# Optimization experiments

Hardware: AMD Instinct MI355X
Metric: run time of the kernel (lower is better)

## Reference

```python
import jax, jax.numpy as jnp
import numpy as np

B, L, D_MODEL = 1, 2048, 1024
D_STATE, D_CONV, EXPAND = 16, 4, 2
D_INNER = EXPAND * D_MODEL          # 2048
DT_RANK = D_MODEL // 16             # 64
I_SIZE = 4 * D_MODEL                # 4096
EPS = 1e-6


def setup_inputs() -> dict:
    key = jax.random.key(0)
    ks = jax.random.split(key, 24)
    s = 0.02
    inp = {
        "hidden_states": jax.random.normal(ks[0], (B, L, D_MODEL), jnp.float32),
        "attention_mask": jnp.ones((B, L), jnp.float32),
        "mnorm_w": jnp.ones((D_MODEL,), jnp.float32),
        "ln1_w": jnp.ones((D_MODEL,), jnp.float32),
        "ln2_w": jnp.ones((D_MODEL,), jnp.float32),
        "gate_w": jax.random.normal(ks[1], (I_SIZE, D_MODEL), jnp.float32) * s,
        "up_w": jax.random.normal(ks[2], (I_SIZE, D_MODEL), jnp.float32) * s,
        "down_w": jax.random.normal(ks[3], (D_MODEL, I_SIZE), jnp.float32) * s,
    }
    a_log = jnp.log(jnp.broadcast_to(jnp.arange(1, D_STATE + 1, dtype=jnp.float32), (D_INNER, D_STATE)))
    i = 4
    for d in ("f", "b"):
        inp[f"in_w_{d}"] = jax.random.normal(ks[i], (2 * D_INNER, D_MODEL), jnp.float32) * s; i += 1
        inp[f"conv_w_{d}"] = jax.random.normal(ks[i], (D_INNER, D_CONV), jnp.float32) * s; i += 1
        inp[f"conv_b_{d}"] = jnp.zeros((D_INNER,), jnp.float32)
        inp[f"xproj_w_{d}"] = jax.random.normal(ks[i], (DT_RANK + 2 * D_STATE, D_INNER), jnp.float32) * s; i += 1
        inp[f"dt_w_{d}"] = jax.random.normal(ks[i], (D_INNER, DT_RANK), jnp.float32) * s; i += 1
        inp[f"dt_b_{d}"] = jax.random.normal(ks[i], (D_INNER,), jnp.float32) * 0.1; i += 1
        inp[f"A_log_{d}"] = a_log
        inp[f"Dp_{d}"] = jnp.ones((D_INNER,), jnp.float32)
        inp[f"out_w_{d}"] = jax.random.normal(ks[i], (D_MODEL, D_INNER), jnp.float32) * s; i += 1
    return inp


def rmsnorm(x, w, eps=EPS):
    xf = x.astype(jnp.float32)
    var = jnp.mean(xf * xf, axis=-1, keepdims=True)
    return w * (xf * jax.lax.rsqrt(var + eps)).astype(x.dtype)


def depthwise_causal_conv(x, w, b):
    # x: [B,L,C], w: [C,K] -> causal depthwise conv, output [B,L,C]
    xt = jnp.transpose(x, (0, 2, 1))                      # [B,C,L]
    k = w[:, None, :]                                     # [C,1,K] (OIL)
    y = jax.lax.conv_general_dilated(
        xt, k, window_strides=(1,), padding=[(D_CONV - 1, 0)],
        dimension_numbers=("NCL", "OIL", "NCL"), feature_group_count=D_INNER)
    return jnp.transpose(y + b[None, :, None], (0, 2, 1))


def selective_scan(u, dt, Bm, Cm, A):
    # u, dt: [B,L,Di]; Bm, Cm: [B,L,N]; A: [Di,N]
    def step(h, inp):
        dt_t, B_t, C_t, u_t = inp                         # [B,Di],[B,N],[B,N],[B,Di]
        dA = jnp.exp(dt_t[:, :, None] * A)                # [B,Di,N]
        h = dA * h + (dt_t * u_t)[:, :, None] * B_t[:, None, :]
        y = jnp.einsum("bdn,bn->bd", h, C_t)
        return h, y
    h0 = jnp.zeros((u.shape[0], A.shape[0], A.shape[1]), u.dtype)
    xs = (jnp.swapaxes(dt, 0, 1), jnp.swapaxes(Bm, 0, 1), jnp.swapaxes(Cm, 0, 1), jnp.swapaxes(u, 0, 1))
    _, ys = jax.lax.scan(step, h0, xs)                    # ys: [L,B,Di]
    return jnp.swapaxes(ys, 0, 1)


def mamba_dir(x, in_w, conv_w, conv_b, xproj_w, dt_w, dt_b, A_log, Dp, out_w):
    xz = x @ in_w.T                                       # [B,L,2*Di]
    xi, z = jnp.split(xz, 2, axis=-1)
    xc = jax.nn.silu(depthwise_causal_conv(xi, conv_w, conv_b))
    dbc = xc @ xproj_w.T                                  # [B,L,dt_rank+2N]
    dt_raw = dbc[..., :DT_RANK]
    Bm = dbc[..., DT_RANK:DT_RANK + D_STATE]
    Cm = dbc[..., DT_RANK + D_STATE:]
    dt = jax.nn.softplus(dt_raw @ dt_w.T + dt_b)          # [B,L,Di]
    A = -jnp.exp(A_log)
    y = selective_scan(xc, dt, Bm, Cm, A) + xc * Dp
    y = y * jax.nn.silu(z)
    return y @ out_w.T


def reference(hidden_states, attention_mask,
              in_w_f, conv_w_f, conv_b_f, xproj_w_f, dt_w_f, dt_b_f, A_log_f, Dp_f, out_w_f,
              in_w_b, conv_w_b, conv_b_b, xproj_w_b, dt_w_b, dt_b_b, A_log_b, Dp_b, out_w_b,
              mnorm_w, ln1_w, ln2_w, gate_w, up_w, down_w):
    x = hidden_states
    h = rmsnorm(x, ln1_w) * attention_mask[..., None]
    y_f = mamba_dir(h, in_w_f, conv_w_f, conv_b_f, xproj_w_f, dt_w_f, dt_b_f, A_log_f, Dp_f, out_w_f)
    y_b = jnp.flip(mamba_dir(jnp.flip(h, axis=1), in_w_b, conv_w_b, conv_b_b, xproj_w_b,
                             dt_w_b, dt_b_b, A_log_b, Dp_b, out_w_b), axis=1)
    x = x + rmsnorm(y_f + y_b, mnorm_w)                   # fuse='add' + block RMSNorm, residual
    h2 = rmsnorm(x, ln2_w)
    mlp = (jax.nn.silu(h2 @ gate_w.T) * (h2 @ up_w.T)) @ down_w.T
    return x + mlp
```

## Files before the change

kernel.cpp:

```cpp
#include <hip/hip_runtime.h>

#define L_SEQ 2048
#define DMODEL 1024
#define DINNER 2048
#define DSTATE 16
#define DTRANK 64
#define DBC_LD 96
#define NC 64
#define TC 32
#define DCAT 4096
#define XZLD 8192
#define LS96 (L_SEQ * 96)

typedef __bf16 bf16x8 __attribute__((ext_vector_type(8)));
typedef __bf16 bf16x4 __attribute__((ext_vector_type(4)));
typedef float f32x4 __attribute__((ext_vector_type(4)));

__device__ __forceinline__ void gload_lds16(const void* g, void* l) {
    __builtin_amdgcn_global_load_lds(
        (const __attribute__((address_space(1))) void*)g,
        (__attribute__((address_space(3))) void*)l, 16, 0, 0);
}

template<int EPI>
__global__ __launch_bounds__(256) void gemm16(
    const __bf16* __restrict__ A, const __bf16* __restrict__ W,
    float* __restrict__ C, const float* __restrict__ aux, __bf16* __restrict__ Cb,
    int M, int N, int K, int lda, int ldb, int ldc, int kSplit)
{
    __shared__ __bf16 lsA[128 * 64];
    __shared__ __bf16 lsB[128 * 64];
    const int tid  = threadIdx.x;
    const int lane = tid & 63;
    const int wave = tid >> 6;
    const int wr = wave >> 1, wc = wave & 1;
    const int m0 = blockIdx.x * 128, n0 = blockIdx.y * 128;
    const int kz = blockIdx.z;
    const int Kc = K / kSplit;
    const int q  = lane & 7;
    const int rb = wave * 32 + (lane >> 3);

    f32x4 acc[4][4] = {};

    for (int k0 = kz * Kc; k0 < kz * Kc + Kc; k0 += 64) {
        #pragma unroll
        for (int i = 0; i < 4; ++i) {
            const int row = rb + i * 8;
            const int sk  = (q * 8) ^ ((row & 7) << 3);
            gload_lds16(A + (size_t)(m0 + row) * lda + k0 + sk,
                        &lsA[(wave * 4 + i) * 512]);
            int rw = n0 + row; rw = rw < N ? rw : N - 1;
            gload_lds16(W + (size_t)rw * ldb + k0 + sk,
                        &lsB[(wave * 4 + i) * 512]);
        }
        __syncthreads();
        #pragma unroll
        for (int kk = 0; kk < 2; ++kk) {
            bf16x8 af[4], bf[4];
            #pragma unroll
            for (int m = 0; m < 4; ++m) {
                const int row = wr * 64 + m * 16 + (lane & 15);
                const int kb  = (kk * 32 + (lane >> 4) * 8) ^ ((row & 7) << 3);
                af[m] = *(const bf16x8*)&lsA[row * 64 + kb];
            }
            #pragma unroll
            for (int n = 0; n < 4; ++n) {
                const int row = wc * 64 + n * 16 + (lane & 15);
                const int kb  = (kk * 32 + (lane >> 4) * 8) ^ ((row & 7) << 3);
                bf[n] = *(const bf16x8*)&lsB[row * 64 + kb];
            }
            #pragma unroll
            for (int m = 0; m < 4; ++m)
            #pragma unroll
            for (int n = 0; n < 4; ++n)
                acc[m][n] = __builtin_amdgcn_mfma_f32_16x16x32_bf16(af[m], bf[n], acc[m][n], 0, 0, 0);
        }
        __syncthreads();
    }

    float* Cout = (EPI == 5) ? C + (size_t)kz * M * ldc : C;
    const int cr = (lane >> 4) * 4, cc = lane & 15;
    #pragma unroll
    for (int mi = 0; mi < 4; ++mi)
    #pragma unroll
    for (int ni = 0; ni < 4; ++ni) {
        const int c = n0 + wc * 64 + ni * 16 + cc;
        if (c >= N) continue;
        #pragma unroll
        for (int g = 0; g < 4; ++g) {
            const int r = m0 + wr * 64 + mi * 16 + cr + g;
            float v = acc[mi][ni][g];
            if (EPI == 1) {
                float xv = v + aux[c];
                Cout[(size_t)r * ldc + c] = (xv > 20.f) ? xv : log1pf(__expf(xv));
            } else if (EPI == 6) {
                const int rr = (c < (N >> 1)) ? r : (M - 1 - r);
                Cb[(size_t)rr * ldc + c] = (__bf16)v;
            } else {
                Cout[(size_t)r * ldc + c] = v;
            }
        }
    }
}

__global__ __launch_bounds__(256) void gemm_mlp(
    const __bf16* __restrict__ A, const __bf16* __restrict__ Wg,
    const __bf16* __restrict__ Wu, __bf16* __restrict__ m16,
    int M, int N, int K, int lda, int ldb, int ldm)
{
    __shared__ __bf16 lsA[128 * 64];
    __shared__ __bf16 lsB[128 * 64];
    const int tid  = threadIdx.x;
    const int lane = tid & 63;
    const int wave = tid >> 6;
    const int wr = wave >> 1, wc = wave & 1;
    const int m0 = blockIdx.x * 128, n0 = blockIdx.y * 64;
    const int q  = lane & 7;
    const int rb = wave * 32 + (lane >> 3);

    f32x4 acc[4][4] = {};

    for (int k0 = 0; k0 < K; k0 += 64) {
        #pragma unroll
        for (int i = 0; i < 4; ++i) {
            const int row = rb + i * 8;
            const int sk  = (q * 8) ^ ((row & 7) << 3);
            gload_lds16(A + (size_t)(m0 + row) * lda + k0 + sk,
                        &lsA[(wave * 4 + i) * 512]);
            const __bf16* src = (row < 64) ? Wg + (size_t)(n0 + row) * ldb
                                           : Wu + (size_t)(n0 + row - 64) * ldb;
            gload_lds16(src + k0 + sk, &lsB[(wave * 4 + i) * 512]);
        }
        __syncthreads();
        #pragma unroll
        for (int kk = 0; kk < 2; ++kk) {
            bf16x8 af[4], bf[4];
            #pragma unroll
            for (int m = 0; m < 4; ++m) {
                const int row = wr * 64 + m * 16 + (lane & 15);
                const int kb  = (kk * 32 + (lane >> 4) * 8) ^ ((row & 7) << 3);
                af[m] = *(const bf16x8*)&lsA[row * 64 + kb];
            }
            #pragma unroll
            for (int n = 0; n < 4; ++n) {
                const int row = wc * 32 + (n & 1) * 16 + (n >> 1) * 64 + (lane & 15);
                const int kb  = (kk * 32 + (lane >> 4) * 8) ^ ((row & 7) << 3);
                bf[n] = *(const bf16x8*)&lsB[row * 64 + kb];
            }
            #pragma unroll
            for (int m = 0; m < 4; ++m)
            #pragma unroll
            for (int n = 0; n < 4; ++n)
                acc[m][n] = __builtin_amdgcn_mfma_f32_16x16x32_bf16(af[m], bf[n], acc[m][n], 0, 0, 0);
        }
        __syncthreads();
    }

    const int cr = (lane >> 4) * 4, cc = lane & 15;
    #pragma unroll
    for (int mi = 0; mi < 4; ++mi)
    #pragma unroll
    for (int nn = 0; nn < 2; ++nn) {
        const int c = n0 + wc * 32 + nn * 16 + cc;
        #pragma unroll
        for (int g = 0; g < 4; ++g) {
            const int r = m0 + wr * 64 + mi * 16 + cr + g;
            const float gv = acc[mi][nn][g];
            const float uv = acc[mi][nn + 2][g];
            m16[(size_t)r * ldm + c] = (__bf16)(gv / (1.f + __expf(-gv)) * uv);
        }
    }
}

#define NJOBS 9
struct CvtJobs {
    const float* src[NJOBS];
    __bf16* dst[NJOBS];
    int cum[NJOBS + 1];
};
__global__ __launch_bounds__(256) void cvt_multi(CvtJobs j, int total8) {
    const int g = blockIdx.x * 256 + threadIdx.x;
    if (g >= total8) return;
    for (int i = 0; i < NJOBS; ++i) {
        if (g < j.cum[i + 1]) {
            const int off = (g - j.cum[i]) * 8;
            const float4 a = *(const float4*)(j.src[i] + off);
            const float4 b = *(const float4*)(j.src[i] + off + 4);
            bf16x8 o;
            o[0]=(__bf16)a.x; o[1]=(__bf16)a.y; o[2]=(__bf16)a.z; o[3]=(__bf16)a.w;
            o[4]=(__bf16)b.x; o[5]=(__bf16)b.y; o[6]=(__bf16)b.z; o[7]=(__bf16)b.w;
            *(bf16x8*)(j.dst[i] + off) = o;
            return;
        }
    }
}

__global__ __launch_bounds__(256) void cvt_outw(
    const float* __restrict__ wf, const float* __restrict__ wb, __bf16* __restrict__ dst)
{
    const int g = blockIdx.x * 256 + threadIdx.x;
    const int half = g >> 18;
    const int i = (g & 262143) * 8;
    const int r = i >> 11, c = i & 2047;
    const float* src = (half ? wb : wf) + (size_t)r * 2048 + c;
    const float4 a = *(const float4*)src;
    const float4 b = *(const float4*)(src + 4);
    bf16x8 o;
    o[0]=(__bf16)a.x; o[1]=(__bf16)a.y; o[2]=(__bf16)a.z; o[3]=(__bf16)a.w;
    o[4]=(__bf16)b.x; o[5]=(__bf16)b.y; o[6]=(__bf16)b.z; o[7]=(__bf16)b.w;
    *(bf16x8*)(dst + (size_t)r * 4096 + half * 2048 + c) = o;
}

__global__ __launch_bounds__(256) void rmsnorm_mask_kernel(
    const float* __restrict__ x, const float* __restrict__ w, const float* __restrict__ mask,
    __bf16* __restrict__ h16)
{
    __shared__ float sred[4];
    const int row = blockIdx.x, t = threadIdx.x;
    float4 v = ((const float4*)(x + (size_t)row * DMODEL))[t];
    float ss = v.x*v.x + v.y*v.y + v.z*v.z + v.w*v.w;
    #pragma unroll
    for (int m = 1; m < 64; m <<= 1) ss += __shfl_xor(ss, m);
    if ((t & 63) == 0) sred[t >> 6] = ss;
    __syncthreads();
    ss = sred[0] + sred[1] + sred[2] + sred[3];
    const float scale = rsqrtf(ss * (1.f / DMODEL) + 1e-6f) * mask[row];
    float4 wv = ((const float4*)w)[t];
    bf16x4 o;
    o[0] = (__bf16)(v.x * wv.x * scale); o[1] = (__bf16)(v.y * wv.y * scale);
    o[2] = (__bf16)(v.z * wv.z * scale); o[3] = (__bf16)(v.w * wv.w * scale);
    *(bf16x4*)&h16[(size_t)row * DMODEL + t * 4] = o;
}

__global__ __launch_bounds__(256) void conv_silu_kernel(
    const __bf16* __restrict__ xz,
    const float* __restrict__ w0, const float* __restrict__ b0,
    const float* __restrict__ w1, const float* __restrict__ b1,
    __bf16* __restrict__ xc16)
{
    const int idx = blockIdx.x * 256 + threadIdx.x;
    const int dcat = idx & (DCAT - 1);
    const int t = idx >> 12;
    const int dir = dcat >> 11, dloc = dcat & 2047;
    const float* w = (dir ? w1 : w0) + dloc * 4;
    float acc = (dir ? b1 : b0)[dloc];
    const float4 wv = *(const float4*)w;
    const float wj[4] = {wv.x, wv.y, wv.z, wv.w};
    const __bf16* src = xz + dir * 4096 + dloc;
    #pragma unroll
    for (int jj = 0; jj < 4; ++jj) {
        const int tt = t - 3 + jj;
        if (tt >= 0) acc += wj[jj] * (float)src[(size_t)tt * XZLD];
    }
    xc16[(size_t)idx] = (__bf16)(acc / (1.f + __expf(-acc)));
}

__global__ __launch_bounds__(256) void dbc_finalize(
    const float* __restrict__ P, float* __restrict__ dbc, __bf16* __restrict__ dbc16)
{
    const int i = blockIdx.x * 256 + threadIdx.x;
    const int dir = i / LS96, rem = i - dir * LS96;
    float v = 0.f;
    #pragma unroll
    for (int s = 0; s < 8; ++s) v += P[(size_t)dir * 8 * LS96 + (size_t)s * LS96 + rem];
    dbc[i] = v;
    const int r = rem / 96, c = rem - r * 96;
    if (c < DTRANK) dbc16[(size_t)dir * L_SEQ * DTRANK + r * DTRANK + c] = (__bf16)v;
}

__global__ __launch_bounds__(256) void scan_p1(
    const __bf16* __restrict__ u, const float* __restrict__ dt,
    const float* __restrict__ dbc, const float* __restrict__ A0, const float* __restrict__ A1,
    __bf16* __restrict__ Pb, __bf16* __restrict__ Sb)
{
    __shared__ float sB[TC * 16];
    const int tid = threadIdx.x;
    const int c = blockIdx.x;
    const int dcat = blockIdx.y * 256 + tid;
    const int dir = blockIdx.y >> 3;
    const int dloc = dcat & 2047;
    const int t0 = c * TC;
    const float* dbcD = dbc + (size_t)dir * LS96;
    for (int i = tid; i < TC * 16; i += 256)
        sB[i] = dbcD[(t0 + (i >> 4)) * DBC_LD + DTRANK + (i & 15)];
    __syncthreads();
    const float* Alog = (dir ? A1 : A0) + (size_t)dloc * 16;
    float A[16], h[16], Pa[16];
    #pragma unroll
    for (int n = 0; n < 16; n += 4) {
        const float4 av = *(const float4*)(Alog + n);
        A[n]   = -__expf(av.x); A[n+1] = -__expf(av.y);
        A[n+2] = -__expf(av.z); A[n+3] = -__expf(av.w);
    }
    #pragma unroll
    for (int n = 0; n < 16; ++n) { h[n] = 0.f; Pa[n] = 1.f; }
    #pragma unroll 2
    for (int t = 0; t < TC; ++t) {
        const float dtv = dt[(size_t)(t0 + t) * DCAT + dcat];
        const float du  = dtv * (float)u[(size_t)(t0 + t) * DCAT + dcat];
        #pragma unroll
        for (int n = 0; n < 16; ++n) {
            const float a = __expf(dtv * A[n]);
            h[n] = a * h[n] + du * sB[t * 16 + n];
            Pa[n] *= a;
        }
    }
    __bf16* pp = Pb + ((size_t)c * DCAT + dcat) * 16;
    __bf16* sp = Sb + ((size_t)c * DCAT + dcat) * 16;
    bf16x8 pv0, pv1, sv0, sv1;
    #pragma unroll
    for (int n = 0; n < 8; ++n) {
        pv0[n] = (__bf16)Pa[n]; pv1[n] = (__bf16)Pa[n + 8];
        sv0[n] = (__bf16)h[n];  sv1[n] = (__bf16)h[n + 8];
    }
    *(bf16x8*)pp = pv0; *(bf16x8*)(pp + 8) = pv1;
    *(bf16x8*)sp = sv0; *(bf16x8*)(sp + 8) = sv1;
}

__global__ __launch_bounds__(256) void scan_mid(
    const __bf16* __restrict__ Pb, const __bf16* __restrict__ Sb, __bf16* __restrict__ Hb)
{
    const int i = blockIdx.x * 256 + threadIdx.x;
    float H = 0.f;
    for (int c = 0; c < NC; ++c) {
        Hb[(size_t)c * 65536 + i] = (__bf16)H;
        H = (float)Pb[(size_t)c * 65536 + i] * H + (float)Sb[(size_t)c * 65536 + i];
    }
}

__global__ __launch_bounds__(256) void scan_p3(
    const __bf16* __restrict__ u, const float* __restrict__ dt,
    const float* __restrict__ dbc, const float* __restrict__ A0, const float* __restrict__ A1,
    const float* __restrict__ Dp0, const float* __restrict__ Dp1,
    const __bf16* __restrict__ Hb, const __bf16* __restrict__ xz,
    __bf16* __restrict__ ygcat)
{
    __shared__ float sB[TC * 16], sC[TC * 16];
    const int tid = threadIdx.x;
    const int c = blockIdx.x;
    const int dcat = blockIdx.y * 256 + tid;
    const int dir = blockIdx.y >> 3;
    const int dloc = dcat & 2047;
    const int t0 = c * TC;
    const float* dbcD = dbc + (size_t)dir * LS96;
    for (int i = tid; i < TC * 16; i += 256) {
        sB[i] = dbcD[(t0 + (i >> 4)) * DBC_LD + DTRANK + (i & 15)];
        sC[i] = dbcD[(t0 + (i >> 4)) * DBC_LD + DTRANK + DSTATE + (i & 15)];
    }
    __syncthreads();
    const float* Alog = (dir ? A1 : A0) + (size_t)dloc * 16;
    const __bf16* hp = Hb + ((size_t)c * DCAT + dcat) * 16;
    const bf16x8 hv0 = *(const bf16x8*)hp;
    const bf16x8 hv1 = *(const bf16x8*)(hp + 8);
    float A[16], h[16];
    #pragma unroll
    for (int n = 0; n < 8; ++n) { h[n] = (float)hv0[n]; h[n + 8] = (float)hv1[n]; }
    #pragma unroll
    for (int n = 0; n < 16; n += 4) {
        const float4 av = *(const float4*)(Alog + n);
        A[n]   = -__expf(av.x); A[n+1] = -__expf(av.y);
        A[n+2] = -__expf(av.z); A[n+3] = -__expf(av.w);
    }
    const float Dv = (dir ? Dp1 : Dp0)[dloc];
    const __bf16* zsrc = xz + dir * 4096 + 2048 + dloc;
    #pragma unroll 2
    for (int t = 0; t < TC; ++t) {
        const float dtv = dt[(size_t)(t0 + t) * DCAT + dcat];
        const float uv  = (float)u[(size_t)(t0 + t) * DCAT + dcat];
        const float du  = dtv * uv;
        float y = uv * Dv;
        #pragma unroll
        for (int n = 0; n < 16; ++n) {
            const float a = __expf(dtv * A[n]);
            h[n] = a * h[n] + du * sB[t * 16 + n];
            y += h[n] * sC[t * 16 + n];
        }
        const float zv = (float)zsrc[(size_t)(t0 + t) * XZLD];
        const int orow = dir ? (L_SEQ - 1 - (t0 + t)) : (t0 + t);
        ygcat[(size_t)orow * DCAT + dcat] = (__bf16)(y * (zv / (1.f + __expf(-zv))));
    }
}

__global__ __launch_bounds__(256) void addnorm2_kernel(
    const float* __restrict__ x0, const float* __restrict__ P,
    const float* __restrict__ mw, const float* __restrict__ w2,
    float* __restrict__ x2, __bf16* __restrict__ h2_16)
{
    __shared__ float sred[8];
    const int row = blockIdx.x, t = threadIdx.x;
    const size_t PS = (size_t)L_SEQ * DMODEL;
    float4 yv = ((const float4*)(P + (size_t)row * DMODEL))[t];
    #pragma unroll
    for (int s = 1; s < 4; ++s) {
        float4 pv = ((const float4*)(P + s * PS + (size_t)row * DMODEL))[t];
        yv.x += pv.x; yv.y += pv.y; yv.z += pv.z; yv.w += pv.w;
    }
    float ss = yv.x*yv.x + yv.y*yv.y + yv.z*yv.z + yv.w*yv.w;
    #pragma unroll
    for (int m = 1; m < 64; m <<= 1) ss += __shfl_xor(ss, m);
    if ((t & 63) == 0) sred[t >> 6] = ss;
    __syncthreads();
    const float s1 = sred[0] + sred[1] + sred[2] + sred[3];
    const float sc1 = rsqrtf(s1 * (1.f / DMODEL) + 1e-6f);
    float4 xv = ((const float4*)(x0 + (size_t)row * DMODEL))[t];
    float4 mv = ((const float4*)mw)[t];
    float4 o;
    o.x = xv.x + mv.x * yv.x * sc1; o.y = xv.y + mv.y * yv.y * sc1;
    o.z = xv.z + mv.z * yv.z * sc1; o.w = xv.w + mv.w * yv.w * sc1;
    ((float4*)(x2 + (size_t)row * DMODEL))[t] = o;
    float s2 = o.x*o.x + o.y*o.y + o.z*o.z + o.w*o.w;
    #pragma unroll
    for (int m = 1; m < 64; m <<= 1) s2 += __shfl_xor(s2, m);
    if ((t & 63) == 0) sred[4 + (t >> 6)] = s2;
    __syncthreads();
    const float st = sred[4] + sred[5] + sred[6] + sred[7];
    const float sc2 = rsqrtf(st * (1.f / DMODEL) + 1e-6f);
    float4 wv = ((const float4*)w2)[t];
    bf16x4 o2;
    o2[0] = (__bf16)(wv.x * o.x * sc2); o2[1] = (__bf16)(wv.y * o.y * sc2);
    o2[2] = (__bf16)(wv.z * o.z * sc2); o2[3] = (__bf16)(wv.w * o.w * sc2);
    *(bf16x4*)&h2_16[(size_t)row * DMODEL + t * 4] = o2;
}

__global__ __launch_bounds__(256) void addout_kernel(
    const float* __restrict__ x2, const float* __restrict__ P, float* __restrict__ out)
{
    const size_t i = ((size_t)blockIdx.x * 256 + threadIdx.x) * 4;
    const size_t PS = (size_t)L_SEQ * DMODEL;
    float4 v = *(const float4*)(x2 + i);
    #pragma unroll
    for (int s = 0; s < 4; ++s) {
        const float4 pv = *(const float4*)(P + s * PS + i);
        v.x += pv.x; v.y += pv.y; v.z += pv.z; v.w += pv.w;
    }
    *(float4*)(out + i) = v;
}

extern "C" void kernel_launch(void* const* d_in, const int* in_sizes, int n_in,
                              void* d_out, int out_size, void* d_ws, size_t ws_size,
                              hipStream_t stream)
{
    const float* x       = (const float*)d_in[0];
    const float* mask    = (const float*)d_in[1];
    const float* mnorm_w = (const float*)d_in[2];
    const float* ln1_w   = (const float*)d_in[3];
    const float* ln2_w   = (const float*)d_in[4];
    const float* gate_w  = (const float*)d_in[5];
    const float* up_w    = (const float*)d_in[6];
    const float* down_w  = (const float*)d_in[7];
    const float* in_w[2]    = {(const float*)d_in[8],  (const float*)d_in[17]};
    const float* conv_w[2]  = {(const float*)d_in[9],  (const float*)d_in[18]};
    const float* conv_b[2]  = {(const float*)d_in[10], (const float*)d_in[19]};
    const float* xproj_w[2] = {(const float*)d_in[11], (const float*)d_in[20]};
    const float* dt_w[2]    = {(const float*)d_in[12], (const float*)d_in[21]};
    const float* dt_b[2]    = {(const float*)d_in[13], (const float*)d_in[22]};
    const float* A_log[2]   = {(const float*)d_in[14], (const float*)d_in[23]};
    const float* Dp[2]      = {(const float*)d_in[15], (const float*)d_in[24]};
    const float* out_w[2]   = {(const float*)d_in[16], (const float*)d_in[25]};

    float* ws = (float*)d_ws;
    const size_t MF = 1u << 20;
    __bf16* h16    = (__bf16*)(ws);
    float*  x2     = ws + 1 * MF;
    __bf16* xzcat  = (__bf16*)(ws + 3 * MF);
    __bf16* xc16   = (__bf16*)(ws + 11 * MF);
    float*  dtb    = ws + 15 * MF;
    float*  dbc    = ws + 23 * MF;
    __bf16* dbc16  = (__bf16*)(ws + 23 * MF + 524288);
    __bf16* Pb     = (__bf16*)(ws + 24 * MF);
    __bf16* Sb     = (__bf16*)(ws + 26 * MF);
    float*  dbcP   = ws + 24 * MF;
    __bf16* Hb     = (__bf16*)(ws + 28 * MF);
    __bf16* ygcat  = (__bf16*)(ws + 30 * MF);
    __bf16* h2_16  = (__bf16*)(ws + 34 * MF);
    __bf16* wbase  = (__bf16*)(ws + 35 * MF);
    const size_t M4 = 4u << 20, M2 = 2u << 20;
    __bf16* wINcat  = wbase;
    __bf16* wOUTcat = wbase + 2 * M4;
    __bf16* wG      = wbase + 3 * M4;
    __bf16* wU      = wbase + 4 * M4;
    __bf16* wDN     = wbase + 5 * M4;
    __bf16* wXP[2]  = {wbase + 6 * M4,            wbase + 6 * M4 + 196608};
    __bf16* wDT[2]  = {wbase + 6 * M4 + 393216,   wbase + 6 * M4 + 524288};
    __bf16* mbuf16  = ygcat;
    float*  gemmP   = dtb;

    CvtJobs j;
    const float* srcs[NJOBS] = {in_w[0], in_w[1], gate_w, up_w, down_w,
                                xproj_w[0], xproj_w[1], dt_w[0], dt_w[1]};
    __bf16* dsts[NJOBS] = {wINcat, wINcat + M4, wG, wU, wDN, wXP[0], wXP[1], wDT[0], wDT[1]};
    const int szs[NJOBS] = {4194304, 4194304, 4194304, 4194304, 4194304,
                            196608, 196608, 131072, 131072};
    int cum = 0;
    for (int i = 0; i < NJOBS; ++i) {
        j.src[i] = srcs[i]; j.dst[i] = dsts[i]; j.cum[i] = cum; cum += szs[i] / 8;
    }
    j.cum[NJOBS] = cum;
    cvt_multi<<<(cum + 255) / 256, 256, 0, stream>>>(j, cum);
    cvt_outw<<<(2 * 1024 * 2048 / 8) / 256, 256, 0, stream>>>(out_w[0], out_w[1], wOUTcat);

    rmsnorm_mask_kernel<<<L_SEQ, 256, 0, stream>>>(x, ln1_w, mask, h16);

    gemm16<6><<<dim3(16, 64), 256, 0, stream>>>(
        h16, wINcat, nullptr, nullptr, xzcat, 2048, 8192, 1024, 1024, 1024, 8192, 1);

    conv_silu_kernel<<<(L_SEQ * DCAT) / 256, 256, 0, stream>>>(
        xzcat, conv_w[0], conv_b[0], conv_w[1], conv_b[1], xc16);

    for (int dir = 0; dir < 2; ++dir)
        gemm16<5><<<dim3(16, 1, 8), 256, 0, stream>>>(
            xc16 + dir * 2048, wXP[dir], dbcP + (size_t)dir * 8 * LS96, nullptr, nullptr,
            2048, 96, 2048, 4096, 2048, 96, 8);
    dbc_finalize<<<(2 * LS96) / 256, 256, 0, stream>>>(dbcP, dbc, dbc16);

    for (int dir = 0; dir < 2; ++dir)
        gemm16<1><<<dim3(16, 16), 256, 0, stream>>>(
            dbc16 + (size_t)dir * L_SEQ * DTRANK, wDT[dir], dtb + dir * 2048, dt_b[dir],
            nullptr, 2048, 2048, 64, 64, 64, 4096, 1);

    scan_p1<<<dim3(NC, 16), 256, 0, stream>>>(
        xc16, dtb, dbc, A_log[0], A_log[1], Pb, Sb);
    scan_mid<<<65536 / 256, 256, 0, stream>>>(Pb, Sb, Hb);
    scan_p3<<<dim3(NC, 16), 256, 0, stream>>>(
        xc16, dtb, dbc, A_log[0], A_log[1], Dp[0], Dp[1], Hb, xzcat, ygcat);

    gemm16<5><<<dim3(16, 8, 4), 256, 0, stream>>>(
        ygcat, wOUTcat, gemmP, nullptr, nullptr, 2048, 1024, 4096, 4096, 4096, 1024, 4);
    addnorm2_kernel<<<L_SEQ, 256, 0, stream>>>(x, gemmP, mnorm_w, ln2_w, x2, h2_16);

    gemm_mlp<<<dim3(16, 64), 256, 0, stream>>>(
        h2_16, wG, wU, mbuf16, 2048, 4096, 1024, 1024, 1024, 4096);
    gemm16<5><<<dim3(16, 8, 4), 256, 0, stream>>>(
        mbuf16, wDN, gemmP, nullptr, nullptr, 2048, 1024, 4096, 4096, 4096, 1024, 4);
    addout_kernel<<<(L_SEQ * DMODEL) / (256 * 4), 256, 0, stream>>>(
        x2, gemmP, (float*)d_out);
}
```

Measured before the change: 384.0 us.

## Split GEMM kernels, add XCD-aware block swizzle, store dt in bf16, merge direction launches

The templated GEMM is split into specialized kernels around a shared core. The in-projection, MLP and split-K partial GEMMs now remap block indices so neighbouring tiles land on the same XCD for better L2 reuse. The per-direction x-proj and dt GEMM launches are merged into single launches using blockIdx.z. The softplus dt output is stored as bf16 instead of fp32, halving scan read traffic at some precision cost. Workspace offsets are rearranged to fit.

```diff
diff --git a/kernel.cpp b/kernel.cpp
--- a/kernel.cpp
+++ b/kernel.cpp
@@ -22,27 +22,27 @@
         (__attribute__((address_space(3))) void*)l, 16, 0, 0);
 }
 
-template<int EPI>
-__global__ __launch_bounds__(256) void gemm16(
+__device__ __forceinline__ void xcd_swz16(int& bx, int& by, int nwg) {
+    const int lin = by * 16 + bx;
+    const int s = (lin & 7) * (nwg >> 3) + (lin >> 3);
+    bx = s & 15;
+    by = s >> 4;
+}
+
+__device__ __forceinline__ void gemm_core(
     const __bf16* __restrict__ A, const __bf16* __restrict__ W,
-    float* __restrict__ C, const float* __restrict__ aux, __bf16* __restrict__ Cb,
-    int M, int N, int K, int lda, int ldb, int ldc, int kSplit)
-{
-    __shared__ __bf16 lsA[128 * 64];
-    __shared__ __bf16 lsB[128 * 64];
+    __bf16* lsA, __bf16* lsB,
+    int m0, int n0, int N, int lda, int ldb, int k0b, int k0e,
+    f32x4 (&acc)[4][4])
+{
     const int tid  = threadIdx.x;
     const int lane = tid & 63;
     const int wave = tid >> 6;
     const int wr = wave >> 1, wc = wave & 1;
-    const int m0 = blockIdx.x * 128, n0 = blockIdx.y * 128;
-    const int kz = blockIdx.z;
-    const int Kc = K / kSplit;
     const int q  = lane & 7;
     const int rb = wave * 32 + (lane >> 3);
 
-    f32x4 acc[4][4] = {};
-
-    for (int k0 = kz * Kc; k0 < kz * Kc + Kc; k0 += 64) {
+    for (int k0 = k0b; k0 < k0e; k0 += 64) {
         #pragma unroll
         for (int i = 0; i < 4; ++i) {
             const int row = rb + i * 8;
@@ -56,7 +56,7 @@
         __syncthreads();
         #pragma unroll
         for (int kk = 0; kk < 2; ++kk) {
-            bf16x8 af[4], bf[4];
+            bf16x8 af[4], bfr[4];
             #pragma unroll
             for (int m = 0; m < 4; ++m) {
                 const int row = wr * 64 + m * 16 + (lane & 15);
@@ -67,38 +67,126 @@
             for (int n = 0; n < 4; ++n) {
                 const int row = wc * 64 + n * 16 + (lane & 15);
                 const int kb  = (kk * 32 + (lane >> 4) * 8) ^ ((row & 7) << 3);
-                bf[n] = *(const bf16x8*)&lsB[row * 64 + kb];
+                bfr[n] = *(const bf16x8*)&lsB[row * 64 + kb];
             }
             #pragma unroll
             for (int m = 0; m < 4; ++m)
             #pragma unroll
             for (int n = 0; n < 4; ++n)
-                acc[m][n] = __builtin_amdgcn_mfma_f32_16x16x32_bf16(af[m], bf[n], acc[m][n], 0, 0, 0);
+                acc[m][n] = __builtin_amdgcn_mfma_f32_16x16x32_bf16(af[m], bfr[n], acc[m][n], 0, 0, 0);
         }
         __syncthreads();
     }
-
-    float* Cout = (EPI == 5) ? C + (size_t)kz * M * ldc : C;
+}
+
+#define EPI_SETUP \
+    const int lane = threadIdx.x & 63; \
+    const int wave = threadIdx.x >> 6; \
+    const int wr = wave >> 1, wc = wave & 1; \
     const int cr = (lane >> 4) * 4, cc = lane & 15;
+
+__global__ __launch_bounds__(256) void k_inproj(
+    const __bf16* __restrict__ A, const __bf16* __restrict__ W, __bf16* __restrict__ Cb,
+    int M, int N, int K, int lda, int ldb, int ldc)
+{
+    __shared__ __bf16 lsA[128 * 64], lsB[128 * 64];
+    int bx = blockIdx.x, by = blockIdx.y;
+    xcd_swz16(bx, by, 1024);
+    const int m0 = bx * 128, n0 = by * 128;
+    f32x4 acc[4][4] = {};
+    gemm_core(A, W, lsA, lsB, m0, n0, N, lda, ldb, 0, K, acc);
+    EPI_SETUP
     #pragma unroll
     for (int mi = 0; mi < 4; ++mi)
     #pragma unroll
     for (int ni = 0; ni < 4; ++ni) {
         const int c = n0 + wc * 64 + ni * 16 + cc;
-        if (c >= N) continue;
         #pragma unroll
         for (int g = 0; g < 4; ++g) {
             const int r = m0 + wr * 64 + mi * 16 + cr + g;
-            float v = acc[mi][ni][g];
-            if (EPI == 1) {
-                float xv = v + aux[c];
-                Cout[(size_t)r * ldc + c] = (xv > 20.f) ? xv : log1pf(__expf(xv));
-            } else if (EPI == 6) {
-                const int rr = (c < (N >> 1)) ? r : (M - 1 - r);
-                Cb[(size_t)rr * ldc + c] = (__bf16)v;
-            } else {
-                Cout[(size_t)r * ldc + c] = v;
-            }
+            const int rr = (c < (N >> 1)) ? r : (M - 1 - r);
+            Cb[(size_t)rr * ldc + c] = (__bf16)acc[mi][ni][g];
+        }
+    }
+}
+
+__global__ __launch_bounds__(256) void k_xproj(
+    const __bf16* __restrict__ A, const __bf16* __restrict__ W0, const __bf16* __restrict__ W1,
+    float* __restrict__ P)
+{
+    __shared__ __bf16 lsA[128 * 64], lsB[128 * 64];
+    const int dir = blockIdx.z >> 3, kz = blockIdx.z & 7;
+    const int m0 = blockIdx.x * 128, n0 = 0;
+    const __bf16* W = dir ? W1 : W0;
+    f32x4 acc[4][4] = {};
+    gemm_core(A + dir * 2048, W, lsA, lsB, m0, n0, 96, 4096, 2048,
+              kz * 256, kz * 256 + 256, acc);
+    float* Cout = P + (size_t)blockIdx.z * LS96;
+    EPI_SETUP
+    #pragma unroll
+    for (int mi = 0; mi < 4; ++mi)
+    #pragma unroll
+    for (int ni = 0; ni < 4; ++ni) {
+        const int c = wc * 64 + ni * 16 + cc;
+        if (c >= 96) continue;
+        #pragma unroll
+        for (int g = 0; g < 4; ++g) {
+            const int r = m0 + wr * 64 + mi * 16 + cr + g;
+            Cout[(size_t)r * 96 + c] = acc[mi][ni][g];
+        }
+    }
+}
+
+__global__ __launch_bounds__(256) void k_dt(
+    const __bf16* __restrict__ A, const __bf16* __restrict__ W0, const __bf16* __restrict__ W1,
+    const float* __restrict__ aux0, const float* __restrict__ aux1,
+    __bf16* __restrict__ Cb)
+{
+    __shared__ __bf16 lsA[128 * 64], lsB[128 * 64];
+    const int dir = blockIdx.z;
+    const int m0 = blockIdx.x * 128, n0 = blockIdx.y * 128;
+    const __bf16* W = dir ? W1 : W0;
+    const float* aux = dir ? aux1 : aux0;
+    f32x4 acc[4][4] = {};
+    gemm_core(A + (size_t)dir * L_SEQ * DTRANK, W, lsA, lsB, m0, n0, 2048, 64, 64, 0, 64, acc);
+    EPI_SETUP
+    #pragma unroll
+    for (int mi = 0; mi < 4; ++mi)
+    #pragma unroll
+    for (int ni = 0; ni < 4; ++ni) {
+        const int c = n0 + wc * 64 + ni * 16 + cc;
+        #pragma unroll
+        for (int g = 0; g < 4; ++g) {
+            const int r = m0 + wr * 64 + mi * 16 + cr + g;
+            const float xv = acc[mi][ni][g] + aux[c];
+            const float sp = (xv > 20.f) ? xv : log1pf(__expf(xv));
+            Cb[(size_t)r * DCAT + dir * 2048 + c] = (__bf16)sp;
+        }
+    }
+}
+
+__global__ __launch_bounds__(256) void k_partial(
+    const __bf16* __restrict__ A, const __bf16* __restrict__ W, float* __restrict__ P,
+    int M, int N, int K, int lda, int ldb, int ldc, int kSplit)
+{
+    __shared__ __bf16 lsA[128 * 64], lsB[128 * 64];
+    int bx = blockIdx.x, by = blockIdx.y;
+    xcd_swz16(bx, by, gridDim.x * gridDim.y);
+    const int m0 = bx * 128, n0 = by * 128;
+    const int Kc = K / kSplit, kz = blockIdx.z;
+    f32x4 acc[4][4] = {};
+    gemm_core(A, W, lsA, lsB, m0, n0, N, lda, ldb, kz * Kc, kz * Kc + Kc, acc);
+    float* Cout = P + (size_t)kz * M * ldc;
+    EPI_SETUP
+    #pragma unroll
+    for (int mi = 0; mi < 4; ++mi)
+    #pragma unroll
+    for (int ni = 0; ni < 4; ++ni) {
+        const int c = n0 + wc * 64 + ni * 16 + cc;
+        #pragma unroll
+        for (int g = 0; g < 4; ++g) {
+            const int r = m0 + wr * 64 + mi * 16 + cr + g;
+            Cout[(size_t)r * ldc + c] = acc[mi][ni][g];
         }
     }
 }
@@ -114,7 +202,9 @@
     const int lane = tid & 63;
     const int wave = tid >> 6;
     const int wr = wave >> 1, wc = wave & 1;
-    const int m0 = blockIdx.x * 128, n0 = blockIdx.y * 64;
+    int bx = blockIdx.x, by = blockIdx.y;
+    xcd_swz16(bx, by, 1024);
+    const int m0 = bx * 128, n0 = by * 64;
     const int q  = lane & 7;
     const int rb = wave * 32 + (lane >> 3);
 
@@ -134,7 +224,7 @@
         __syncthreads();
         #pragma unroll
         for (int kk = 0; kk < 2; ++kk) {
-            bf16x8 af[4], bf[4];
+            bf16x8 af[4], bfr[4];
             #pragma unroll
             for (int m = 0; m < 4; ++m) {
                 const int row = wr * 64 + m * 16 + (lane & 15);
@@ -145,13 +235,13 @@
             for (int n = 0; n < 4; ++n) {
                 const int row = wc * 32 + (n & 1) * 16 + (n >> 1) * 64 + (lane & 15);
                 const int kb  = (kk * 32 + (lane >> 4) * 8) ^ ((row & 7) << 3);
-                bf[n] = *(const bf16x8*)&lsB[row * 64 + kb];
+                bfr[n] = *(const bf16x8*)&lsB[row * 64 + kb];
             }
             #pragma unroll
             for (int m = 0; m < 4; ++m)
             #pragma unroll
             for (int n = 0; n < 4; ++n)
-                acc[m][n] = __builtin_amdgcn_mfma_f32_16x16x32_bf16(af[m], bf[n], acc[m][n], 0, 0, 0);
+                acc[m][n] = __builtin_amdgcn_mfma_f32_16x16x32_bf16(af[m], bfr[n], acc[m][n], 0, 0, 0);
         }
         __syncthreads();
     }
@@ -269,7 +359,7 @@
 }
 
 __global__ __launch_bounds__(256) void scan_p1(
-    const __bf16* __restrict__ u, const float* __restrict__ dt,
+    const __bf16* __restrict__ u, const __bf16* __restrict__ dt,
     const float* __restrict__ dbc, const float* __restrict__ A0, const float* __restrict__ A1,
     __bf16* __restrict__ Pb, __bf16* __restrict__ Sb)
 {
@@ -296,7 +386,7 @@
     for (int n = 0; n < 16; ++n) { h[n] = 0.f; Pa[n] = 1.f; }
     #pragma unroll 2
     for (int t = 0; t < TC; ++t) {
-        const float dtv = dt[(size_t)(t0 + t) * DCAT + dcat];
+        const float dtv = (float)dt[(size_t)(t0 + t) * DCAT + dcat];
         const float du  = dtv * (float)u[(size_t)(t0 + t) * DCAT + dcat];
         #pragma unroll
         for (int n = 0; n < 16; ++n) {
@@ -329,7 +419,7 @@
 }
 
 __global__ __launch_bounds__(256) void scan_p3(
-    const __bf16* __restrict__ u, const float* __restrict__ dt,
+    const __bf16* __restrict__ u, const __bf16* __restrict__ dt,
     const float* __restrict__ dbc, const float* __restrict__ A0, const float* __restrict__ A1,
     const float* __restrict__ Dp0, const float* __restrict__ Dp1,
     const __bf16* __restrict__ Hb, const __bf16* __restrict__ xz,
@@ -365,7 +455,7 @@
     const __bf16* zsrc = xz + dir * 4096 + 2048 + dloc;
     #pragma unroll 2
     for (int t = 0; t < TC; ++t) {
-        const float dtv = dt[(size_t)(t0 + t) * DCAT + dcat];
+        const float dtv = (float)dt[(size_t)(t0 + t) * DCAT + dcat];
         const float uv  = (float)u[(size_t)(t0 + t) * DCAT + dcat];
         const float du  = dtv * uv;
         float y = uv * Dv;
@@ -464,17 +554,18 @@
     float*  x2     = ws + 1 * MF;
     __bf16* xzcat  = (__bf16*)(ws + 3 * MF);
     __bf16* xc16   = (__bf16*)(ws + 11 * MF);
-    float*  dtb    = ws + 15 * MF;
-    float*  dbc    = ws + 23 * MF;
-    __bf16* dbc16  = (__bf16*)(ws + 23 * MF + 524288);
+    __bf16* dtb16  = (__bf16*)(ws + 15 * MF);
+    float*  dbc    = ws + 19 * MF;
+    __bf16* dbc16  = (__bf16*)(ws + 19 * MF + 393216);
+    float*  dbcP   = ws + 20 * MF;
     __bf16* Pb     = (__bf16*)(ws + 24 * MF);
     __bf16* Sb     = (__bf16*)(ws + 26 * MF);
-    float*  dbcP   = ws + 24 * MF;
     __bf16* Hb     = (__bf16*)(ws + 28 * MF);
+    float*  gemmP  = ws + 20 * MF;
     __bf16* ygcat  = (__bf16*)(ws + 30 * MF);
     __bf16* h2_16  = (__bf16*)(ws + 34 * MF);
     __bf16* wbase  = (__bf16*)(ws + 35 * MF);
-    const size_t M4 = 4u << 20, M2 = 2u << 20;
+    const size_t M4 = 4u << 20;
     __bf16* wINcat  = wbase;
     __bf16* wOUTcat = wbase + 2 * M4;
     __bf16* wG      = wbase + 3 * M4;
@@ -483,7 +574,6 @@
     __bf16* wXP[2]  = {wbase + 6 * M4,            wbase + 6 * M4 + 196608};
     __bf16* wDT[2]  = {wbase + 6 * M4 + 393216,   wbase + 6 * M4 + 524288};
     __bf16* mbuf16  = ygcat;
-    float*  gemmP   = dtb;
 
     CvtJobs j;
     const float* srcs[NJOBS] = {in_w[0], in_w[1], gate_w, up_w, down_w,
@@ -501,37 +591,32 @@
 
     rmsnorm_mask_kernel<<<L_SEQ, 256, 0, stream>>>(x, ln1_w, mask, h16);
 
-    gemm16<6><<<dim3(16, 64), 256, 0, stream>>>(
-        h16, wINcat, nullptr, nullptr, xzcat, 2048, 8192, 1024, 1024, 1024, 8192, 1);
+    k_inproj<<<dim3(16, 64), 256, 0, stream>>>(
+        h16, wINcat, xzcat, 2048, 8192, 1024, 1024, 1024, 8192);
 
     conv_silu_kernel<<<(L_SEQ * DCAT) / 256, 256, 0, stream>>>(
         xzcat, conv_w[0], conv_b[0], conv_w[1], conv_b[1], xc16);
 
-    for (int dir = 0; dir < 2; ++dir)
-        gemm16<5><<<dim3(16, 1, 8), 256, 0, stream>>>(
-            xc16 + dir * 2048, wXP[dir], dbcP + (size_t)dir * 8 * LS96, nullptr, nullptr,
-            2048, 96, 2048, 4096, 2048, 96, 8);
+    k_xproj<<<dim3(16, 1, 16), 256, 0, stream>>>(xc16, wXP[0], wXP[1], dbcP);
     dbc_finalize<<<(2 * LS96) / 256, 256, 0, stream>>>(dbcP, dbc, dbc16);
 
-    for (int dir = 0; dir < 2; ++dir)
-        gemm16<1><<<dim3(16, 16), 256, 0, stream>>>(
-            dbc16 + (size_t)dir * L_SEQ * DTRANK, wDT[dir], dtb + dir * 2048, dt_b[dir],
-            nullptr, 2048, 2048, 64, 64, 64, 4096, 1);
+    k_dt<<<dim3(16, 16, 2), 256, 0, stream>>>(
+        dbc16, wDT[0], wDT[1], dt_b[0], dt_b[1], dtb16);
 
     scan_p1<<<dim3(NC, 16), 256, 0, stream>>>(
-        xc16, dtb, dbc, A_log[0], A_log[1], Pb, Sb);
+        xc16, dtb16, dbc, A_log[0], A_log[1], Pb, Sb);
     scan_mid<<<65536 / 256, 256, 0, stream>>>(Pb, Sb, Hb);
     scan_p3<<<dim3(NC, 16), 256, 0, stream>>>(
-        xc16, dtb, dbc, A_log[0], A_log[1], Dp[0], Dp[1], Hb, xzcat, ygcat);
-
-    gemm16<5><<<dim3(16, 8, 4), 256, 0, stream>>>(
-        ygcat, wOUTcat, gemmP, nullptr, nullptr, 2048, 1024, 4096, 4096, 4096, 1024, 4);
+        xc16, dtb16, dbc, A_log[0], A_log[1], Dp[0], Dp[1], Hb, xzcat, ygcat);
+
+    k_partial<<<dim3(16, 8, 4), 256, 0, stream>>>(
+        ygcat, wOUTcat, gemmP, 2048, 1024, 4096, 4096, 4096, 1024, 4);
     addnorm2_kernel<<<L_SEQ, 256, 0, stream>>>(x, gemmP, mnorm_w, ln2_w, x2, h2_16);
 
     gemm_mlp<<<dim3(16, 64), 256, 0, stream>>>(
         h2_16, wG, wU, mbuf16, 2048, 4096, 1024, 1024, 1024, 4096);
-    gemm16<5><<<dim3(16, 8, 4), 256, 0, stream>>>(
-        mbuf16, wDN, gemmP, nullptr, nullptr, 2048, 1024, 4096, 4096, 4096, 1024, 4);
+    k_partial<<<dim3(16, 8, 4), 256, 0, stream>>>(
+        mbuf16, wDN, gemmP, 2048, 1024, 4096, 4096, 4096, 1024, 4);
     addout_kernel<<<(L_SEQ * DMODEL) / (256 * 4), 256, 0, stream>>>(
         x2, gemmP, (float*)d_out);
 }
```

Result: faster. 359.3 us (-6.4%).
